# Optimization experiments

Measured on AMD Instinct MI355X. Metric: run time of the kernel, lower is better.

Reference implementation:

```python
import jax, jax.numpy as jnp
import numpy as np

# Model dims
B, N, T = 2, 32, 256
D_MODEL = 128          # d_slow
D_STATE = 16
N_LAYERS = 2
EXPAND = 2
D_INNER = EXPAND * D_MODEL   # 256
D_CONV = 4
DT_RANK = (D_MODEL + 15) // 16  # 8


def setup_inputs() -> dict:
    key = jax.random.key(0)
    ks = jax.random.split(key, 8)
    s = lambda k, shape, scale: jax.random.normal(k, shape, jnp.float32) * scale
    return {
        "x": jax.random.normal(ks[0], (B, N, T, D_MODEL), jnp.float32),
        "in_proj_w": s(ks[1], (N_LAYERS, D_MODEL, 2 * D_INNER), 0.05),
        "conv_w": s(ks[2], (N_LAYERS, D_INNER, 1, D_CONV), 0.2),   # depthwise conv kernels
        "conv_b": jnp.zeros((N_LAYERS, D_INNER), jnp.float32),
        "x_proj_w": s(ks[3], (N_LAYERS, D_INNER, DT_RANK + 2 * D_STATE), 0.05),
        "dt_proj_w": s(ks[4], (N_LAYERS, DT_RANK, D_INNER), 0.1),
        "dt_proj_b": jnp.full((N_LAYERS, D_INNER), -4.0, jnp.float32),  # softplus(-4) ~ small dt
        # slow-timescale init: A_log = log(U(0.001, 0.1)) so A = -exp(A_log) is a weak decay
        "A_log": jnp.log(jax.random.uniform(ks[5], (N_LAYERS, D_INNER, D_STATE),
                                            minval=1e-3, maxval=0.1)),
        "D_param": jnp.ones((N_LAYERS, D_INNER), jnp.float32),
        "out_proj_w": s(ks[6], (N_LAYERS, D_INNER, D_MODEL), 0.05),
    }


def _selective_scan(u, delta, A, Bm, Cm, Dp):
    # u, delta: [b, t, d]; A: [d, n]; Bm, Cm: [b, t, n]; Dp: [d]
    deltaA = jnp.exp(jnp.einsum('btd,dn->btdn', delta, A))          # [b,t,d,n]
    deltaBu = jnp.einsum('btd,btn->btdn', delta * u, Bm)            # [b,t,d,n]
    # time-major for scan
    dA_t = jnp.transpose(deltaA, (1, 0, 2, 3))
    dBu_t = jnp.transpose(deltaBu, (1, 0, 2, 3))
    c_t = jnp.transpose(Cm, (1, 0, 2))

    def step(h, xs):
        dA, dBu, c = xs
        h = dA * h + dBu                                            # [b,d,n]
        y = jnp.einsum('bdn,bn->bd', h, c)
        return h, y

    h0 = jnp.zeros(u.shape[:1] + (u.shape[-1], A.shape[-1]), u.dtype)
    _, ys = jax.lax.scan(step, h0, (dA_t, dBu_t, c_t))              # ys: [t,b,d]
    y = jnp.transpose(ys, (1, 0, 2))
    return y + u * Dp


def _mamba_block(h, in_w, cw, cb, xw, dtw, dtb, A_log, Dp, ow):
    # h: [b, t, d_model]
    xz = h @ in_w                                                   # [b,t,2*d_inner]
    u, res = jnp.split(xz, 2, axis=-1)
    # causal depthwise conv over time
    u_nch = jnp.transpose(u, (0, 2, 1))                             # [b,d_inner,t]
    u_conv = jax.lax.conv_general_dilated(
        u_nch, cw, window_strides=(1,), padding=[(D_CONV - 1, 0)],
        dimension_numbers=('NCH', 'OIH', 'NCH'), feature_group_count=D_INNER)
    u = jax.nn.silu(jnp.transpose(u_conv + cb[None, :, None], (0, 2, 1)))
    # input-dependent dt, B, C
    dbl = u @ xw                                                    # [b,t,dt_rank+2n]
    dt, Bm, Cm = jnp.split(dbl, [DT_RANK, DT_RANK + D_STATE], axis=-1)
    delta = jax.nn.softplus(dt @ dtw + dtb)                         # [b,t,d_inner]
    A = -jnp.exp(A_log)                                             # [d_inner, n]
    y = _selective_scan(u, delta, A, Bm, Cm, Dp)
    return (y * jax.nn.silu(res)) @ ow


def reference(x, in_proj_w, conv_w, conv_b, x_proj_w, dt_proj_w, dt_proj_b,
              A_log, D_param, out_proj_w):
    b, n, t, d = x.shape
    h = x.reshape(b * n, t, d)
    for l in range(N_LAYERS):
        h = _mamba_block(h, in_proj_w[l], conv_w[l], conv_b[l], x_proj_w[l],
                         dt_proj_w[l], dt_proj_b[l], A_log[l], D_param[l],
                         out_proj_w[l])
    return h.reshape(b, n, t, d)
```

## Files before the change

kernel.cpp:

```cpp
#include <hip/hip_runtime.h>
#include <math.h>

#define BT 64
#define T 256
#define DM 128
#define DI 256
#define DS 16
#define DR 8
#define M_ROWS (BT*T)
#define NC 16
#define CL (T/NC)
#define SSZ (BT*DI*DS)

typedef __attribute__((ext_vector_type(8))) short short8v;
typedef __attribute__((ext_vector_type(4))) float f32x4;
typedef __attribute__((ext_vector_type(4))) unsigned int uint4v;
union U8 { unsigned int u[4]; uint4v v; short8v s; };

__device__ __forceinline__ float fast_silu(float x) {
  return x * __builtin_amdgcn_rcpf(1.0f + __expf(-x));
}
__device__ __forceinline__ float softplus_f(float x) {
  return fmaxf(x, 0.0f) + __logf(1.0f + __expf(-fabsf(x)));
}

__device__ __forceinline__ void split3(const float* x, short8v& o1, short8v& o2, short8v& o3) {
  unsigned int h1[8], h2[8], h3[8];
#pragma unroll
  for (int e = 0; e < 8; e++) {
    const float xe = x[e];
    const unsigned int a = __float_as_uint(xe) & 0xFFFF0000u;
    const float r1 = xe - __uint_as_float(a);
    const unsigned int b = __float_as_uint(r1) & 0xFFFF0000u;
    const float r2 = r1 - __uint_as_float(b);
    const unsigned int c = __float_as_uint(r2) & 0xFFFF0000u;
    h1[e] = a; h2[e] = b; h3[e] = c;
  }
  U8 u1, u2, u3;
#pragma unroll
  for (int q = 0; q < 4; q++) {
    u1.u[q] = (h1[2 * q] >> 16) | (h1[2 * q + 1] & 0xFFFF0000u);
    u2.u[q] = (h2[2 * q] >> 16) | (h2[2 * q + 1] & 0xFFFF0000u);
    u3.u[q] = (h3[2 * q] >> 16) | (h3[2 * q + 1] & 0xFFFF0000u);
  }
  o1 = u1.s; o2 = u2.s; o3 = u3.s;
}

__global__ __launch_bounds__(64) void prep_all(
    const float* __restrict__ in_w, const float* __restrict__ xw,
    const float* __restrict__ dtw, const float* __restrict__ ow,
    unsigned int* __restrict__ pw1, unsigned int* __restrict__ pwb,
    unsigned int* __restrict__ pow_) {
  const int b = blockIdx.x;
  const int l = threadIdx.x;
  const int rA = l & 15, kg = l >> 4;
  float x[8];
  unsigned int* dst;
  size_t base;
  if (b < 256) {
    const int layer = b >> 7, rem = b & 127;
    const int ks = rem >> 5, cf = rem & 31;
    const int col = cf * 16 + rA, k0 = ks * 32 + kg * 8;
    const float* W = in_w + (size_t)layer * 128 * 512;
#pragma unroll
    for (int e = 0; e < 8; e++) x[e] = W[(size_t)(k0 + e) * 512 + col];
    dst = pw1 + (size_t)layer * 98304;
    base = (((size_t)ks * 32 + cf) * 64 + l) * 4;
    short8v p1, p2, p3; split3(x, p1, p2, p3);
    U8 t;
    t.s = p1; *reinterpret_cast<uint4v*>(dst + base) = t.v;
    t.s = p2; *reinterpret_cast<uint4v*>(dst + 32768 + base) = t.v;
    t.s = p3; *reinterpret_cast<uint4v*>(dst + 65536 + base) = t.v;
  } else if (b < 576) {
    const int bb = b - 256;
    const int layer = bb / 160, rem = bb % 160;
    const int ks = rem / 20, cf = rem % 20;
    const int col = cf * 16 + rA, k0 = ks * 32 + kg * 8;
    const float* xwl = xw + (size_t)layer * DI * 40;
    const float* dtwl = dtw + (size_t)layer * DR * DI;
#pragma unroll
    for (int e = 0; e < 8; e++) {
      const int k = k0 + e;
      float v = 0.f;
      if (col < 256) {
#pragma unroll
        for (int r = 0; r < DR; r++) v += xwl[k * 40 + r] * dtwl[r * DI + col];
      } else if (col < 288) {
        v = xwl[k * 40 + 8 + (col - 256)];
      }
      x[e] = v;
    }
    dst = pwb + (size_t)layer * 122880;
    base = (((size_t)ks * 20 + cf) * 64 + l) * 4;
    short8v p1, p2, p3; split3(x, p1, p2, p3);
    U8 t;
    t.s = p1; *reinterpret_cast<uint4v*>(dst + base) = t.v;
    t.s = p2; *reinterpret_cast<uint4v*>(dst + 40960 + base) = t.v;
    t.s = p3; *reinterpret_cast<uint4v*>(dst + 81920 + base) = t.v;
  } else {
    const int bb = b - 576;
    const int layer = bb >> 6, rem = bb & 63;
    const int ks = rem >> 3, cf = rem & 7;
    const int col = cf * 16 + rA, k0 = ks * 32 + kg * 8;
    const float* W = ow + (size_t)layer * 256 * 128;
#pragma unroll
    for (int e = 0; e < 8; e++) x[e] = W[(size_t)(k0 + e) * 128 + col];
    dst = pow_ + (size_t)layer * 49152;
    base = (((size_t)ks * 8 + cf) * 64 + l) * 4;
    short8v p1, p2, p3; split3(x, p1, p2, p3);
    U8 t;
    t.s = p1; *reinterpret_cast<uint4v*>(dst + base) = t.v;
    t.s = p2; *reinterpret_cast<uint4v*>(dst + 16384 + base) = t.v;
    t.s = p3; *reinterpret_cast<uint4v*>(dst + 32768 + base) = t.v;
  }
}

template <int FR, int CF, int EPI>
__global__ __launch_bounds__(256, 2) void gemm_mfma(
    const float* __restrict__ A, const unsigned int* __restrict__ Bp,
    float* __restrict__ C, float* __restrict__ Bb, float* __restrict__ Cb,
    const float* __restrict__ dtb, int M, int Nn, int K) {
  const int NWC = Nn / (16 * CF);
  const int wid = blockIdx.x * 4 + (threadIdx.x >> 6);
  const int l = threadIdx.x & 63;
  const int mw = wid / NWC, nw = wid % NWC;
  const int wr0 = mw * (16 * FR), wc0 = nw * (16 * CF);
  const int rA = l & 15, kg = l >> 4;
  const int NF = Nn / 16, Kt = K >> 5;

  f32x4 acc[FR][CF];
#pragma unroll
  for (int fr = 0; fr < FR; fr++)
#pragma unroll
    for (int j = 0; j < CF; j++) acc[fr][j] = (f32x4){0.f, 0.f, 0.f, 0.f};

  for (int ks = 0; ks < Kt; ks++) {
    short8v bf[3][CF];
#pragma unroll
    for (int p = 0; p < 3; p++)
#pragma unroll
      for (int j = 0; j < CF; j++) {
        U8 t;
        t.v = *reinterpret_cast<const uint4v*>(
            Bp + ((((size_t)p * Kt + ks) * NF + (wc0 >> 4) + j) * 64 + l) * 4);
        bf[p][j] = t.s;
      }
    short8v a1[FR], a2[FR], a3[FR];
#pragma unroll
    for (int fr = 0; fr < FR; fr++) {
      const float* ap = A + (size_t)(wr0 + fr * 16 + rA) * K + ks * 32 + kg * 8;
      float x[8];
      *reinterpret_cast<float4*>(x) = *reinterpret_cast<const float4*>(ap);
      *reinterpret_cast<float4*>(x + 4) = *reinterpret_cast<const float4*>(ap + 4);
      split3(x, a1[fr], a2[fr], a3[fr]);
    }
#pragma unroll
    for (int fr = 0; fr < FR; fr++)
#pragma unroll
      for (int j = 0; j < CF; j++) {
        f32x4 c = acc[fr][j];
        c = __builtin_amdgcn_mfma_f32_16x16x32_bf16(a1[fr], bf[0][j], c, 0, 0, 0);
        c = __builtin_amdgcn_mfma_f32_16x16x32_bf16(a1[fr], bf[1][j], c, 0, 0, 0);
        c = __builtin_amdgcn_mfma_f32_16x16x32_bf16(a2[fr], bf[0][j], c, 0, 0, 0);
        c = __builtin_amdgcn_mfma_f32_16x16x32_bf16(a1[fr], bf[2][j], c, 0, 0, 0);
        c = __builtin_amdgcn_mfma_f32_16x16x32_bf16(a3[fr], bf[0][j], c, 0, 0, 0);
        c = __builtin_amdgcn_mfma_f32_16x16x32_bf16(a2[fr], bf[1][j], c, 0, 0, 0);
        acc[fr][j] = c;
      }
  }

  const int cr = (l >> 4) * 4;
  const int cc = l & 15;
  if (EPI == 0) {
#pragma unroll
    for (int fr = 0; fr < FR; fr++)
#pragma unroll
      for (int j = 0; j < CF; j++) {
        const int col = wc0 + j * 16 + cc;
#pragma unroll
        for (int r = 0; r < 4; r++)
          C[(size_t)(wr0 + fr * 16 + cr + r) * Nn + col] = acc[fr][j][r];
      }
  } else {
#pragma unroll
    for (int fr = 0; fr < FR; fr++)
#pragma unroll
      for (int j = 0; j < CF; j++) {
        const int col = wc0 + j * 16 + cc;
        if (col < 256) {
          const float bias = dtb[col];
#pragma unroll
          for (int r = 0; r < 4; r++)
            C[(size_t)(wr0 + fr * 16 + cr + r) * DI + col] =
                softplus_f(acc[fr][j][r] + bias);
        } else if (col < 272) {
#pragma unroll
          for (int r = 0; r < 4; r++)
            Bb[(size_t)(wr0 + fr * 16 + cr + r) * DS + (col - 256)] = acc[fr][j][r];
        } else if (col < 288) {
#pragma unroll
          for (int r = 0; r < 4; r++)
            Cb[(size_t)(wr0 + fr * 16 + cr + r) * DS + (col - 272)] = acc[fr][j][r];
        }
      }
  }
}

__global__ __launch_bounds__(256) void conv_silu_kernel(
    const float* __restrict__ xzr, float* __restrict__ xzw,
    const float* __restrict__ cw, const float* __restrict__ cb,
    float* __restrict__ u) {
  const int d = threadIdx.x;
  const int m0 = blockIdx.x * 8;
  const int t0 = m0 & (T - 1);
  const float4 cv = *reinterpret_cast<const float4*>(&cw[d * 4]);
  const float bias = cb[d];
  float w0 = 0.f, w1 = 0.f, w2 = 0.f;
  if (t0 != 0) {
    w0 = xzr[(size_t)(m0 - 3) * 512 + d];
    w1 = xzr[(size_t)(m0 - 2) * 512 + d];
    w2 = xzr[(size_t)(m0 - 1) * 512 + d];
  }
#pragma unroll
  for (int i = 0; i < 8; i++) {
    const size_t m = m0 + i;
    const float cur = xzr[m * 512 + d];
    const float a = bias + cv.x * w0 + cv.y * w1 + cv.z * w2 + cv.w * cur;
    u[m * DI + d] = fast_silu(a);
    const float r = xzr[m * 512 + 256 + d];
    xzw[m * 512 + 256 + d] = fast_silu(r);
    w0 = w1; w1 = w2; w2 = cur;
  }
}

__global__ __launch_bounds__(256) void scan_phase1(
    const float* __restrict__ delta, const float* __restrict__ u,
    const float* __restrict__ Bb, const float* __restrict__ A_log,
    float* __restrict__ Pb, float* __restrict__ H) {
  const int c  = blockIdx.x;
  const int bt = blockIdx.y;
  const int d  = threadIdx.x;

  float An[16];
  const float4* al = reinterpret_cast<const float4*>(&A_log[d * DS]);
#pragma unroll
  for (int q = 0; q < 4; q++) {
    float4 a = al[q];
    An[q * 4 + 0] = -__expf(a.x);
    An[q * 4 + 1] = -__expf(a.y);
    An[q * 4 + 2] = -__expf(a.z);
    An[q * 4 + 3] = -__expf(a.w);
  }

  float h[16];
#pragma unroll
  for (int n = 0; n < 16; n++) h[n] = 0.f;
  float Sdl = 0.f;

  const size_t m0 = (size_t)bt * T + c * CL;
  for (int t = 0; t < CL; t++) {
    const size_t m = m0 + t;
    const float dl = delta[m * DI + d];
    const float uu = u[m * DI + d];
    const float du = dl * uu;
    Sdl += dl;
    const float4* bp = reinterpret_cast<const float4*>(&Bb[m * DS]);
    const float4 B0 = bp[0], B1 = bp[1], B2 = bp[2], B3 = bp[3];
    const float Bv[16] = {B0.x, B0.y, B0.z, B0.w, B1.x, B1.y, B1.z, B1.w,
                          B2.x, B2.y, B2.z, B2.w, B3.x, B3.y, B3.z, B3.w};
#pragma unroll
    for (int n = 0; n < 16; n++) {
      const float dA = __expf(dl * An[n]);
      h[n] = dA * h[n] + du * Bv[n];
    }
  }

  const size_t idx = ((size_t)c * BT + bt) * 4096 + (size_t)d * 16;
#pragma unroll
  for (int q = 0; q < 4; q++) {
    float4 hv = {h[q * 4 + 0], h[q * 4 + 1], h[q * 4 + 2], h[q * 4 + 3]};
    *reinterpret_cast<float4*>(&H[idx + q * 4]) = hv;
  }
#pragma unroll
  for (int q = 0; q < 4; q++) {
    float4 pv = {__expf(An[q * 4 + 0] * Sdl), __expf(An[q * 4 + 1] * Sdl),
                 __expf(An[q * 4 + 2] * Sdl), __expf(An[q * 4 + 3] * Sdl)};
    *reinterpret_cast<float4*>(&Pb[idx + q * 4]) = pv;
  }
}

__global__ __launch_bounds__(256) void scan_phase2(
    const float* __restrict__ Pb, float* __restrict__ H) {
  const size_t i = (size_t)blockIdx.x * 256 + threadIdx.x;
  float hin = 0.f;
#pragma unroll
  for (int c = 0; c < NC; c++) {
    const size_t idx = (size_t)c * SSZ + i;
    const float Pv = Pb[idx];
    const float Hv = H[idx];
    H[idx] = hin;
    hin = Pv * hin + Hv;
  }
}

__global__ __launch_bounds__(256) void scan_phase3(
    const float* __restrict__ delta, const float* __restrict__ u,
    const float* __restrict__ Bb, const float* __restrict__ Cb,
    const float* __restrict__ xz,
    const float* __restrict__ A_log, const float* __restrict__ Dp,
    const float* __restrict__ H, float* __restrict__ g) {
  const int c  = blockIdx.x;
  const int bt = blockIdx.y;
  const int d  = threadIdx.x;

  float An[16];
  const float4* al = reinterpret_cast<const float4*>(&A_log[d * DS]);
#pragma unroll
  for (int q = 0; q < 4; q++) {
    float4 a = al[q];
    An[q * 4 + 0] = -__expf(a.x);
    An[q * 4 + 1] = -__expf(a.y);
    An[q * 4 + 2] = -__expf(a.z);
    An[q * 4 + 3] = -__expf(a.w);
  }
  const float Dpd = Dp[d];

  float h[16];
  const size_t idx = ((size_t)c * BT + bt) * 4096 + (size_t)d * 16;
#pragma unroll
  for (int q = 0; q < 4; q++) {
    float4 hv = *reinterpret_cast<const float4*>(&H[idx + q * 4]);
    h[q * 4 + 0] = hv.x; h[q * 4 + 1] = hv.y; h[q * 4 + 2] = hv.z; h[q * 4 + 3] = hv.w;
  }

  const size_t m0 = (size_t)bt * T + c * CL;
  for (int t = 0; t < CL; t++) {
    const size_t m = m0 + t;
    const float dl = delta[m * DI + d];
    const float uu = u[m * DI + d];
    const float du = dl * uu;
    const float4* bp = reinterpret_cast<const float4*>(&Bb[m * DS]);
    const float4 B0 = bp[0], B1 = bp[1], B2 = bp[2], B3 = bp[3];
    const float4* cp = reinterpret_cast<const float4*>(&Cb[m * DS]);
    const float4 C0 = cp[0], C1 = cp[1], C2 = cp[2], C3 = cp[3];
    const float Bv[16] = {B0.x, B0.y, B0.z, B0.w, B1.x, B1.y, B1.z, B1.w,
                          B2.x, B2.y, B2.z, B2.w, B3.x, B3.y, B3.z, B3.w};
    const float Cv[16] = {C0.x, C0.y, C0.z, C0.w, C1.x, C1.y, C1.z, C1.w,
                          C2.x, C2.y, C2.z, C2.w, C3.x, C3.y, C3.z, C3.w};
    float y = 0.f;
#pragma unroll
    for (int n = 0; n < 16; n++) {
      const float dA = __expf(dl * An[n]);
      h[n] = dA * h[n] + du * Bv[n];
      y += h[n] * Cv[n];
    }
    const float rs = xz[m * 512 + 256 + d];
    g[m * DI + d] = (y + uu * Dpd) * rs;
  }
}

extern "C" void kernel_launch(void* const* d_in, const int* in_sizes, int n_in,
                              void* d_out, int out_size, void* d_ws, size_t ws_size,
                              hipStream_t stream) {
  const float* x      = (const float*)d_in[0];
  const float* in_w   = (const float*)d_in[1];
  const float* conv_w = (const float*)d_in[2];
  const float* conv_b = (const float*)d_in[3];
  const float* xw     = (const float*)d_in[4];
  const float* dtw    = (const float*)d_in[5];
  const float* dtb    = (const float*)d_in[6];
  const float* A_log  = (const float*)d_in[7];
  const float* Dp     = (const float*)d_in[8];
  const float* ow     = (const float*)d_in[9];
  float* out = (float*)d_out;
  float* ws  = (float*)d_ws;

  float* xz = ws;
  float* u  = ws + 8388608;
  float* dg = ws + 12582912;
  float* Bb = ws + 16777216;
  float* Cb = ws + 17039360;
  float* hb = ws + 17301504;
  float* Hb = ws + 19398656;
  float* Pb = ws + 23592960;
  unsigned int* pl_w1 = (unsigned int*)(ws + 27787264);
  unsigned int* pl_wb = (unsigned int*)(ws + 27983872);
  unsigned int* pl_ow = (unsigned int*)(ws + 28229632);

  prep_all<<<704, 64, 0, stream>>>(in_w, xw, dtw, ow, pl_w1, pl_wb, pl_ow);

  for (int l = 0; l < 2; l++) {
    const float* Ain = (l == 0) ? x : hb;
    float* dst = (l == 1) ? out : hb;

    gemm_mfma<4, 2, 0><<<1024, 256, 0, stream>>>(
        Ain, pl_w1 + (size_t)l * 98304, xz, nullptr, nullptr, nullptr,
        M_ROWS, 512, 128);

    conv_silu_kernel<<<M_ROWS / 8, 256, 0, stream>>>(
        xz, xz, conv_w + (size_t)l * DI * 4, conv_b + (size_t)l * DI, u);

    gemm_mfma<4, 2, 1><<<640, 256, 0, stream>>>(
        u, pl_wb + (size_t)l * 122880, dg, Bb, Cb, dtb + (size_t)l * DI,
        M_ROWS, 320, 256);

    scan_phase1<<<dim3(NC, BT), 256, 0, stream>>>(
        dg, u, Bb, A_log + (size_t)l * DI * DS, Pb, Hb);

    scan_phase2<<<SSZ / 256, 256, 0, stream>>>(Pb, Hb);

    scan_phase3<<<dim3(NC, BT), 256, 0, stream>>>(
        dg, u, Bb, Cb, xz, A_log + (size_t)l * DI * DS, Dp + (size_t)l * DI,
        Hb, dg);

    gemm_mfma<2, 2, 0><<<512, 256, 0, stream>>>(
        dg, pl_ow + (size_t)l * 49152, dst, nullptr, nullptr, nullptr,
        M_ROWS, 128, 256);
  }
}
```

Measured before the change: 277.3 us.

## Pre-split GEMM A operands into bf16 triplets in producer kernels

The three-way bf16 split of the GEMM A operand moves out of the MFMA inner loop. The input is split by a new split_mat kernel, and u and the gated scan output are split in the epilogues of conv_silu and scan_phase3, which write three bf16 planes. The GEMM then loads the pre-split shorts directly and raises its occupancy hint from 2 to 4. This removes the repeated split ALU work per column tile, but adds an extra kernel launch and 1.5x the bytes for A planes, plus scattered 2-byte stores in the producers.

```diff
diff --git a/kernel.cpp b/kernel.cpp
--- a/kernel.cpp
+++ b/kernel.cpp
@@ -44,6 +44,33 @@
     u3.u[q] = (h3[2 * q] >> 16) | (h3[2 * q + 1] & 0xFFFF0000u);
   }
   o1 = u1.s; o2 = u2.s; o3 = u3.s;
+}
+
+__device__ __forceinline__ void split3s(float x, unsigned short& s1,
+                                        unsigned short& s2, unsigned short& s3) {
+  const unsigned int a = __float_as_uint(x) & 0xFFFF0000u;
+  const float r1 = x - __uint_as_float(a);
+  const unsigned int b = __float_as_uint(r1) & 0xFFFF0000u;
+  const float r2 = r1 - __uint_as_float(b);
+  s1 = a >> 16;
+  s2 = b >> 16;
+  s3 = __float_as_uint(r2) >> 16;
+}
+
+__global__ __launch_bounds__(256) void split_mat(
+    const float* __restrict__ A, unsigned int* __restrict__ P, int MKdiv8) {
+  const int i = blockIdx.x * 256 + threadIdx.x;
+  if (i >= MKdiv8) return;
+  float x[8];
+  *reinterpret_cast<float4*>(x) = *reinterpret_cast<const float4*>(A + (size_t)i * 8);
+  *reinterpret_cast<float4*>(x + 4) = *reinterpret_cast<const float4*>(A + (size_t)i * 8 + 4);
+  short8v p1, p2, p3;
+  split3(x, p1, p2, p3);
+  const size_t ps = (size_t)MKdiv8 * 4;
+  U8 t;
+  t.s = p1; *reinterpret_cast<uint4v*>(P + (size_t)i * 4) = t.v;
+  t.s = p2; *reinterpret_cast<uint4v*>(P + ps + (size_t)i * 4) = t.v;
+  t.s = p3; *reinterpret_cast<uint4v*>(P + 2 * ps + (size_t)i * 4) = t.v;
 }
 
 __global__ __launch_bounds__(64) void prep_all(
@@ -116,8 +143,8 @@
 }
 
 template <int FR, int CF, int EPI>
-__global__ __launch_bounds__(256, 2) void gemm_mfma(
-    const float* __restrict__ A, const unsigned int* __restrict__ Bp,
+__global__ __launch_bounds__(256, 4) void gemm_mfma(
+    const unsigned short* __restrict__ Ap, const unsigned int* __restrict__ Bp,
     float* __restrict__ C, float* __restrict__ Bb, float* __restrict__ Cb,
     const float* __restrict__ dtb, int M, int Nn, int K) {
   const int NWC = Nn / (16 * CF);
@@ -127,6 +154,7 @@
   const int wr0 = mw * (16 * FR), wc0 = nw * (16 * CF);
   const int rA = l & 15, kg = l >> 4;
   const int NF = Nn / 16, Kt = K >> 5;
+  const size_t AP = (size_t)M * K;
 
   f32x4 acc[FR][CF];
 #pragma unroll
@@ -145,28 +173,24 @@
             Bp + ((((size_t)p * Kt + ks) * NF + (wc0 >> 4) + j) * 64 + l) * 4);
         bf[p][j] = t.s;
       }
-    short8v a1[FR], a2[FR], a3[FR];
 #pragma unroll
     for (int fr = 0; fr < FR; fr++) {
-      const float* ap = A + (size_t)(wr0 + fr * 16 + rA) * K + ks * 32 + kg * 8;
-      float x[8];
-      *reinterpret_cast<float4*>(x) = *reinterpret_cast<const float4*>(ap);
-      *reinterpret_cast<float4*>(x + 4) = *reinterpret_cast<const float4*>(ap + 4);
-      split3(x, a1[fr], a2[fr], a3[fr]);
-    }
-#pragma unroll
-    for (int fr = 0; fr < FR; fr++)
+      const unsigned short* ap = Ap + (size_t)(wr0 + fr * 16 + rA) * K + ks * 32 + kg * 8;
+      const short8v a1 = *reinterpret_cast<const short8v*>(ap);
+      const short8v a2 = *reinterpret_cast<const short8v*>(ap + AP);
+      const short8v a3 = *reinterpret_cast<const short8v*>(ap + 2 * AP);
 #pragma unroll
       for (int j = 0; j < CF; j++) {
         f32x4 c = acc[fr][j];
-        c = __builtin_amdgcn_mfma_f32_16x16x32_bf16(a1[fr], bf[0][j], c, 0, 0, 0);
-        c = __builtin_amdgcn_mfma_f32_16x16x32_bf16(a1[fr], bf[1][j], c, 0, 0, 0);
-        c = __builtin_amdgcn_mfma_f32_16x16x32_bf16(a2[fr], bf[0][j], c, 0, 0, 0);
-        c = __builtin_amdgcn_mfma_f32_16x16x32_bf16(a1[fr], bf[2][j], c, 0, 0, 0);
-        c = __builtin_amdgcn_mfma_f32_16x16x32_bf16(a3[fr], bf[0][j], c, 0, 0, 0);
-        c = __builtin_amdgcn_mfma_f32_16x16x32_bf16(a2[fr], bf[1][j], c, 0, 0, 0);
+        c = __builtin_amdgcn_mfma_f32_16x16x32_bf16(a1, bf[0][j], c, 0, 0, 0);
+        c = __builtin_amdgcn_mfma_f32_16x16x32_bf16(a1, bf[1][j], c, 0, 0, 0);
+        c = __builtin_amdgcn_mfma_f32_16x16x32_bf16(a2, bf[0][j], c, 0, 0, 0);
+        c = __builtin_amdgcn_mfma_f32_16x16x32_bf16(a1, bf[2][j], c, 0, 0, 0);
+        c = __builtin_amdgcn_mfma_f32_16x16x32_bf16(a3, bf[0][j], c, 0, 0, 0);
+        c = __builtin_amdgcn_mfma_f32_16x16x32_bf16(a2, bf[1][j], c, 0, 0, 0);
         acc[fr][j] = c;
       }
+    }
   }
 
   const int cr = (l >> 4) * 4;
@@ -209,7 +233,7 @@
 __global__ __launch_bounds__(256) void conv_silu_kernel(
     const float* __restrict__ xzr, float* __restrict__ xzw,
     const float* __restrict__ cw, const float* __restrict__ cb,
-    float* __restrict__ u) {
+    float* __restrict__ u, unsigned short* __restrict__ au) {
   const int d = threadIdx.x;
   const int m0 = blockIdx.x * 8;
   const int t0 = m0 & (T - 1);
@@ -226,7 +250,14 @@
     const size_t m = m0 + i;
     const float cur = xzr[m * 512 + d];
     const float a = bias + cv.x * w0 + cv.y * w1 + cv.z * w2 + cv.w * cur;
-    u[m * DI + d] = fast_silu(a);
+    const float uv = fast_silu(a);
+    u[m * DI + d] = uv;
+    unsigned short s1, s2, s3;
+    split3s(uv, s1, s2, s3);
+    const size_t pi = m * DI + d;
+    au[pi] = s1;
+    au[(size_t)M_ROWS * DI + pi] = s2;
+    au[2 * (size_t)M_ROWS * DI + pi] = s3;
     const float r = xzr[m * 512 + 256 + d];
     xzw[m * 512 + 256 + d] = fast_silu(r);
     w0 = w1; w1 = w2; w2 = cur;
@@ -308,7 +339,7 @@
     const float* __restrict__ Bb, const float* __restrict__ Cb,
     const float* __restrict__ xz,
     const float* __restrict__ A_log, const float* __restrict__ Dp,
-    const float* __restrict__ H, float* __restrict__ g) {
+    const float* __restrict__ H, unsigned short* __restrict__ ag) {
   const int c  = blockIdx.x;
   const int bt = blockIdx.y;
   const int d  = threadIdx.x;
@@ -355,7 +386,13 @@
       y += h[n] * Cv[n];
     }
     const float rs = xz[m * 512 + 256 + d];
-    g[m * DI + d] = (y + uu * Dpd) * rs;
+    const float gv = (y + uu * Dpd) * rs;
+    unsigned short s1, s2, s3;
+    split3s(gv, s1, s2, s3);
+    const size_t pi = m * DI + d;
+    ag[pi] = s1;
+    ag[(size_t)M_ROWS * DI + pi] = s2;
+    ag[2 * (size_t)M_ROWS * DI + pi] = s3;
   }
 }
 
@@ -386,6 +423,9 @@
   unsigned int* pl_w1 = (unsigned int*)(ws + 27787264);
   unsigned int* pl_wb = (unsigned int*)(ws + 27983872);
   unsigned int* pl_ow = (unsigned int*)(ws + 28229632);
+  unsigned int* ax    = (unsigned int*)(ws + 28327936);
+  unsigned short* au  = (unsigned short*)(ws + 31473664);
+  unsigned short* ag  = (unsigned short*)(ws + 37765120);
 
   prep_all<<<704, 64, 0, stream>>>(in_w, xw, dtw, ow, pl_w1, pl_wb, pl_ow);
 
@@ -393,15 +433,17 @@
     const float* Ain = (l == 0) ? x : hb;
     float* dst = (l == 1) ? out : hb;
 
+    split_mat<<<1024, 256, 0, stream>>>(Ain, ax, M_ROWS * DM / 8);
+
     gemm_mfma<4, 2, 0><<<1024, 256, 0, stream>>>(
-        Ain, pl_w1 + (size_t)l * 98304, xz, nullptr, nullptr, nullptr,
-        M_ROWS, 512, 128);
+        (const unsigned short*)ax, pl_w1 + (size_t)l * 98304, xz,
+        nullptr, nullptr, nullptr, M_ROWS, 512, 128);
 
     conv_silu_kernel<<<M_ROWS / 8, 256, 0, stream>>>(
-        xz, xz, conv_w + (size_t)l * DI * 4, conv_b + (size_t)l * DI, u);
+        xz, xz, conv_w + (size_t)l * DI * 4, conv_b + (size_t)l * DI, u, au);
 
     gemm_mfma<4, 2, 1><<<640, 256, 0, stream>>>(
-        u, pl_wb + (size_t)l * 122880, dg, Bb, Cb, dtb + (size_t)l * DI,
+        au, pl_wb + (size_t)l * 122880, dg, Bb, Cb, dtb + (size_t)l * DI,
         M_ROWS, 320, 256);
 
     scan_phase1<<<dim3(NC, BT), 256, 0, stream>>>(
@@ -411,10 +453,10 @@
 
     scan_phase3<<<dim3(NC, BT), 256, 0, stream>>>(
         dg, u, Bb, Cb, xz, A_log + (size_t)l * DI * DS, Dp + (size_t)l * DI,
-        Hb, dg);
+        Hb, ag);
 
     gemm_mfma<2, 2, 0><<<512, 256, 0, stream>>>(
-        dg, pl_ow + (size_t)l * 49152, dst, nullptr, nullptr, nullptr,
+        ag, pl_ow + (size_t)l * 49152, dst, nullptr, nullptr, nullptr,
         M_ROWS, 128, 256);
   }
 }
```

Result: slower. 328.4 us (+18.4%).

## Fuse gate SiLU into in_proj GEMM epilogue and retile GEMMs with XCD-aware block mapping

Applied to the files above, without the earlier changes.

Moves the SiLU on the gate half of the in_proj output from the conv kernel into a new GEMM epilogue, so the conv kernel no longer reads and rewrites that half of xz. The GEMMs are retiled from 4x2 or 2x2 fragment tiles per wave to 1x4, with occupancy raised to 4 blocks per CU. A block-index swizzle (blockIdx & 7) spreads consecutive tiles across the XCDs. Smaller per-wave tiles cut register pressure but reduce reuse of the B fragments across rows.

```diff
diff --git a/kernel.cpp b/kernel.cpp
--- a/kernel.cpp
+++ b/kernel.cpp
@@ -116,12 +116,13 @@
 }
 
 template <int FR, int CF, int EPI>
-__global__ __launch_bounds__(256, 2) void gemm_mfma(
-    const float* __restrict__ A, const unsigned int* __restrict__ Bp,
+__global__ __launch_bounds__(256, 4) void gemm_mfma(
+    const float* __restrict__ Af, const unsigned int* __restrict__ Bp,
     float* __restrict__ C, float* __restrict__ Bb, float* __restrict__ Cb,
-    const float* __restrict__ dtb, int M, int Nn, int K) {
+    const float* __restrict__ dtb, int M, int Nn, int K, int cpx) {
   const int NWC = Nn / (16 * CF);
-  const int wid = blockIdx.x * 4 + (threadIdx.x >> 6);
+  const int tile = (blockIdx.x & 7) * cpx + (blockIdx.x >> 3);
+  const int wid = tile * 4 + (threadIdx.x >> 6);
   const int l = threadIdx.x & 63;
   const int mw = wid / NWC, nw = wid % NWC;
   const int wr0 = mw * (16 * FR), wc0 = nw * (16 * CF);
@@ -145,28 +146,26 @@
             Bp + ((((size_t)p * Kt + ks) * NF + (wc0 >> 4) + j) * 64 + l) * 4);
         bf[p][j] = t.s;
       }
-    short8v a1[FR], a2[FR], a3[FR];
 #pragma unroll
     for (int fr = 0; fr < FR; fr++) {
-      const float* ap = A + (size_t)(wr0 + fr * 16 + rA) * K + ks * 32 + kg * 8;
+      const float* ap = Af + (size_t)(wr0 + fr * 16 + rA) * K + ks * 32 + kg * 8;
       float x[8];
       *reinterpret_cast<float4*>(x) = *reinterpret_cast<const float4*>(ap);
       *reinterpret_cast<float4*>(x + 4) = *reinterpret_cast<const float4*>(ap + 4);
-      split3(x, a1[fr], a2[fr], a3[fr]);
-    }
-#pragma unroll
-    for (int fr = 0; fr < FR; fr++)
+      short8v a1, a2, a3;
+      split3(x, a1, a2, a3);
 #pragma unroll
       for (int j = 0; j < CF; j++) {
         f32x4 c = acc[fr][j];
-        c = __builtin_amdgcn_mfma_f32_16x16x32_bf16(a1[fr], bf[0][j], c, 0, 0, 0);
-        c = __builtin_amdgcn_mfma_f32_16x16x32_bf16(a1[fr], bf[1][j], c, 0, 0, 0);
-        c = __builtin_amdgcn_mfma_f32_16x16x32_bf16(a2[fr], bf[0][j], c, 0, 0, 0);
-        c = __builtin_amdgcn_mfma_f32_16x16x32_bf16(a1[fr], bf[2][j], c, 0, 0, 0);
-        c = __builtin_amdgcn_mfma_f32_16x16x32_bf16(a3[fr], bf[0][j], c, 0, 0, 0);
-        c = __builtin_amdgcn_mfma_f32_16x16x32_bf16(a2[fr], bf[1][j], c, 0, 0, 0);
+        c = __builtin_amdgcn_mfma_f32_16x16x32_bf16(a1, bf[0][j], c, 0, 0, 0);
+        c = __builtin_amdgcn_mfma_f32_16x16x32_bf16(a1, bf[1][j], c, 0, 0, 0);
+        c = __builtin_amdgcn_mfma_f32_16x16x32_bf16(a2, bf[0][j], c, 0, 0, 0);
+        c = __builtin_amdgcn_mfma_f32_16x16x32_bf16(a1, bf[2][j], c, 0, 0, 0);
+        c = __builtin_amdgcn_mfma_f32_16x16x32_bf16(a3, bf[0][j], c, 0, 0, 0);
+        c = __builtin_amdgcn_mfma_f32_16x16x32_bf16(a2, bf[1][j], c, 0, 0, 0);
         acc[fr][j] = c;
       }
+    }
   }
 
   const int cr = (l >> 4) * 4;
@@ -181,7 +180,7 @@
         for (int r = 0; r < 4; r++)
           C[(size_t)(wr0 + fr * 16 + cr + r) * Nn + col] = acc[fr][j][r];
       }
-  } else {
+  } else if (EPI == 1) {
 #pragma unroll
     for (int fr = 0; fr < FR; fr++)
 #pragma unroll
@@ -203,11 +202,27 @@
             Cb[(size_t)(wr0 + fr * 16 + cr + r) * DS + (col - 272)] = acc[fr][j][r];
         }
       }
+  } else {
+#pragma unroll
+    for (int fr = 0; fr < FR; fr++)
+#pragma unroll
+      for (int j = 0; j < CF; j++) {
+        const int col = wc0 + j * 16 + cc;
+        if (col < 256) {
+#pragma unroll
+          for (int r = 0; r < 4; r++)
+            C[(size_t)(wr0 + fr * 16 + cr + r) * Nn + col] = acc[fr][j][r];
+        } else {
+#pragma unroll
+          for (int r = 0; r < 4; r++)
+            C[(size_t)(wr0 + fr * 16 + cr + r) * Nn + col] = fast_silu(acc[fr][j][r]);
+        }
+      }
   }
 }
 
 __global__ __launch_bounds__(256) void conv_silu_kernel(
-    const float* __restrict__ xzr, float* __restrict__ xzw,
+    const float* __restrict__ xzr,
     const float* __restrict__ cw, const float* __restrict__ cb,
     float* __restrict__ u) {
   const int d = threadIdx.x;
@@ -227,8 +242,6 @@
     const float cur = xzr[m * 512 + d];
     const float a = bias + cv.x * w0 + cv.y * w1 + cv.z * w2 + cv.w * cur;
     u[m * DI + d] = fast_silu(a);
-    const float r = xzr[m * 512 + 256 + d];
-    xzw[m * 512 + 256 + d] = fast_silu(r);
     w0 = w1; w1 = w2; w2 = cur;
   }
 }
@@ -393,16 +406,16 @@
     const float* Ain = (l == 0) ? x : hb;
     float* dst = (l == 1) ? out : hb;
 
-    gemm_mfma<4, 2, 0><<<1024, 256, 0, stream>>>(
-        Ain, pl_w1 + (size_t)l * 98304, xz, nullptr, nullptr, nullptr,
-        M_ROWS, 512, 128);
+    gemm_mfma<1, 4, 3><<<2048, 256, 0, stream>>>(
+        Ain, pl_w1 + (size_t)l * 98304, xz,
+        nullptr, nullptr, nullptr, M_ROWS, 512, 128, 256);
 
     conv_silu_kernel<<<M_ROWS / 8, 256, 0, stream>>>(
-        xz, xz, conv_w + (size_t)l * DI * 4, conv_b + (size_t)l * DI, u);
-
-    gemm_mfma<4, 2, 1><<<640, 256, 0, stream>>>(
+        xz, conv_w + (size_t)l * DI * 4, conv_b + (size_t)l * DI, u);
+
+    gemm_mfma<1, 4, 1><<<1280, 256, 0, stream>>>(
         u, pl_wb + (size_t)l * 122880, dg, Bb, Cb, dtb + (size_t)l * DI,
-        M_ROWS, 320, 256);
+        M_ROWS, 320, 256, 160);
 
     scan_phase1<<<dim3(NC, BT), 256, 0, stream>>>(
         dg, u, Bb, A_log + (size_t)l * DI * DS, Pb, Hb);
@@ -413,8 +426,8 @@
         dg, u, Bb, Cb, xz, A_log + (size_t)l * DI * DS, Dp + (size_t)l * DI,
         Hb, dg);
 
-    gemm_mfma<2, 2, 0><<<512, 256, 0, stream>>>(
+    gemm_mfma<1, 4, 0><<<512, 256, 0, stream>>>(
         dg, pl_ow + (size_t)l * 49152, dst, nullptr, nullptr, nullptr,
-        M_ROWS, 128, 256);
-  }
-}
+        M_ROWS, 128, 256, 64);
+  }
+}
```

New measurement: 256.4 us. -7.5%, faster.
